# Performance work log

Measured on AMD Instinct MI355X. Metric: run time of the kernel, lower is better.

## Reference

```python
import jax, jax.numpy as jnp
import numpy as np

HEADS = 8
DIM_HEAD = 40
LN_EPS = 1e-5


def setup_inputs() -> dict:
    key = jax.random.key(0)
    ks = jax.random.split(key, 6)
    b, c, h, w = 8, 320, 64, 64
    ctx_len, ctx_dim = 77, 768
    inner = HEADS * DIM_HEAD  # 320
    return {
        "x": jax.random.normal(ks[0], (b, c, h, w), jnp.float32),
        "context": jax.random.normal(ks[1], (b, ctx_len, ctx_dim), jnp.float32),
        "Wq": jax.random.normal(ks[2], (c, inner), jnp.float32) * 0.02,
        "Wk": jax.random.normal(ks[3], (ctx_dim, inner), jnp.float32) * 0.02,
        "Wv": jax.random.normal(ks[4], (ctx_dim, inner), jnp.float32) * 0.02,
        "Wout": jax.random.normal(ks[5], (inner, c), jnp.float32) * 0.02,
        "bout": jnp.zeros((c,), jnp.float32),
        "gamma": jnp.ones((c,), jnp.float32),
        "beta": jnp.zeros((c,), jnp.float32),
    }


def reference(x, context, Wq, Wk, Wv, Wout, bout, gamma, beta):
    b, c, h, w = x.shape
    n = h * w
    scale = DIM_HEAD ** -0.5
    # flatten spatial -> tokens: [b, n, c]
    x_flat = x.reshape(b, c, n).transpose(0, 2, 1)
    # LayerNorm over channel dim
    mu = jnp.mean(x_flat, axis=-1, keepdims=True)
    var = jnp.mean((x_flat - mu) ** 2, axis=-1, keepdims=True)
    x_norm = (x_flat - mu) / jnp.sqrt(var + LN_EPS) * gamma + beta
    # projections (no bias), split heads: [b, h, n, d]
    def split_heads(t):
        bb, nn, _ = t.shape
        return t.reshape(bb, nn, HEADS, DIM_HEAD).transpose(0, 2, 1, 3)
    q = split_heads(x_norm @ Wq)
    k = split_heads(context @ Wk)
    v = split_heads(context @ Wv)
    sim = jnp.einsum("bhid,bhjd->bhij", q, k) * scale  # [b,H,n,ctx]
    attn = jax.nn.softmax(sim, axis=-1)
    out = jnp.einsum("bhij,bhjd->bhid", attn, v)
    out = out.transpose(0, 2, 1, 3).reshape(b, n, HEADS * DIM_HEAD)
    out = out @ Wout + bout  # dropout is identity at inference
    out = out + x_flat
    return out.transpose(0, 2, 1).reshape(b, c, h, w)
```

## Files before the change

kernel.cpp:

```cpp
#include <hip/hip_runtime.h>

#define HEADS 8
#define DH 40
constexpr int Bn   = 8;
constexpr int Cc   = 320;
constexpr int Nn   = 4096;
constexpr int CTX  = 77;
constexpr float LN_EPS = 1e-5f;
constexpr float SCALE  = 0.15811388300841897f;

typedef short bf16x8 __attribute__((ext_vector_type(8)));
typedef float f32x4  __attribute__((ext_vector_type(4)));
typedef unsigned short us;

__device__ inline us f2bf(float f) {
    unsigned u = __float_as_uint(f);
    u += 0x7fffu + ((u >> 16) & 1u);
    return (us)(u >> 16);
}
__device__ inline float bf2f(us h) {
    return __uint_as_float(((unsigned)h) << 16);
}

__global__ __launch_bounds__(256) void wtrans_all(const float* __restrict__ Wq,
                                                  const float* __restrict__ Wk,
                                                  const float* __restrict__ Wv,
                                                  const float* __restrict__ Wout,
                                                  us* __restrict__ wqF,
                                                  us* __restrict__ WkT,
                                                  us* __restrict__ WvT,
                                                  us* __restrict__ WoutT) {
    int id = blockIdx.x;
    if (id >= 580) {
        int wid = (id - 580) * 4 + (threadIdx.x >> 6);
        int lane = threadIdx.x & 63, lr = lane & 15, g = lane >> 4;
        int ct = wid / 10, kc = wid % 10;
        int k0 = kc * 32 + g * 8, co = ct * 16 + lr;
        us tmp[8];
        #pragma unroll
        for (int e = 0; e < 8; ++e)
            tmp[e] = f2bf(Wq[(size_t)(k0 + e) * 320 + co]);
        ((uint4*)wqF)[(size_t)wid * 64 + lane] = *(uint4*)tmp;
        return;
    }
    const float* in; us* out; int K, t;
    if (id < 240)      { in = Wk;   out = WkT;   K = 768; t = id; }
    else if (id < 480) { in = Wv;   out = WvT;   K = 768; t = id - 240; }
    else               { in = Wout; out = WoutT; K = 320; t = id - 480; }
    int ktiles = K >> 5;
    int kb = (t % ktiles) * 32, ob = (t / ktiles) * 32;

    __shared__ float tile[32][33];
    int tx = threadIdx.x & 31, ty = threadIdx.x >> 5;
    #pragma unroll
    for (int i = 0; i < 32; i += 8)
        tile[ty + i][tx] = in[(size_t)(kb + ty + i) * 320 + ob + tx];
    __syncthreads();
    #pragma unroll
    for (int i = 0; i < 32; i += 8)
        out[(size_t)(ob + ty + i) * K + kb + tx] = f2bf(tile[tx][ty + i]);
}

__global__ __launch_bounds__(256, 3) void ln_q_fused(const float* __restrict__ x,
                                                     const float* __restrict__ gamma,
                                                     const float* __restrict__ beta,
                                                     const us* __restrict__ wqF,
                                                     us* __restrict__ qG) {
    __shared__ __align__(16) us xnt[64 * 328];
    __shared__ float red1[4][64], red2[4][64];
    __shared__ float mu_s[64], rs_s[64];

    int b  = blockIdx.x >> 6;
    int t0 = (blockIdx.x & 63) * 64;
    int tid = threadIdx.x;
    int tl = tid & 63, cg = tid >> 6;
    const float* xb = x + (size_t)b * Cc * Nn + t0 + tl;

    float s1 = 0.f, s2 = 0.f;
    #pragma unroll 8
    for (int i = 0; i < 80; ++i) {
        int c = cg * 80 + i;
        float v = xb[(size_t)c * Nn];
        s1 += v; s2 += v * v;
        xnt[tl * 328 + c] = f2bf(v);
    }
    red1[cg][tl] = s1; red2[cg][tl] = s2;
    __syncthreads();
    if (tid < 64) {
        float a1 = red1[0][tl] + red1[1][tl] + red1[2][tl] + red1[3][tl];
        float a2 = red2[0][tl] + red2[1][tl] + red2[2][tl] + red2[3][tl];
        float mu = a1 * (1.0f / Cc);
        float var = a2 * (1.0f / Cc) - mu * mu;
        mu_s[tl] = mu; rs_s[tl] = rsqrtf(var + LN_EPS);
    }
    __syncthreads();
    float mu = mu_s[tl], rs = rs_s[tl];
    #pragma unroll 4
    for (int i = 0; i < 40; ++i) {
        int c = cg * 80 + i * 2;
        unsigned u = *(unsigned*)&xnt[tl * 328 + c];
        float v0 = bf2f((us)(u & 0xffff));
        float v1 = bf2f((us)(u >> 16));
        unsigned lo = f2bf((v0 - mu) * rs * gamma[c]     + beta[c]);
        unsigned hi = f2bf((v1 - mu) * rs * gamma[c + 1] + beta[c + 1]);
        *(unsigned*)&xnt[tl * 328 + c] = lo | (hi << 16);
    }
    __syncthreads();

    int lane = tid & 63, w = tid >> 6;
    int lr = lane & 15, g = lane >> 4;
    f32x4 acc[4][5] = {};
    const bf16x8* wq = (const bf16x8*)wqF;
    for (int kc = 0; kc < 10; ++kc) {
        bf16x8 bfr[5];
        #pragma unroll
        for (int nt = 0; nt < 5; ++nt)
            bfr[nt] = wq[(size_t)((w * 5 + nt) * 10 + kc) * 64 + lane];
        bf16x8 afr[4];
        #pragma unroll
        for (int mt = 0; mt < 4; ++mt)
            afr[mt] = *(const bf16x8*)&xnt[(mt * 16 + lr) * 328 + kc * 32 + g * 8];
        #pragma unroll
        for (int mt = 0; mt < 4; ++mt)
            #pragma unroll
            for (int nt = 0; nt < 5; ++nt)
                acc[mt][nt] = __builtin_amdgcn_mfma_f32_16x16x32_bf16(afr[mt], bfr[nt], acc[mt][nt], 0, 0, 0);
    }
    __syncthreads();

    #pragma unroll
    for (int mt = 0; mt < 4; ++mt)
        #pragma unroll
        for (int nt = 0; nt < 5; ++nt)
            #pragma unroll
            for (int r = 0; r < 4; ++r)
                xnt[(mt * 16 + g * 4 + r) * 328 + w * 80 + nt * 16 + lr] = f2bf(acc[mt][nt][r]);
    __syncthreads();

    size_t gtb = (size_t)b * 256 + (blockIdx.x & 63) * 4;
    #pragma unroll
    for (int it = 0; it < 10; ++it) {
        int f_lin = it * 4 + w;
        int tile = f_lin / 10, f = f_lin % 10;
        uint4 v = *(uint4*)&xnt[(tile * 16 + lr) * 328 + f * 32 + g * 8];
        ((uint4*)qG)[((gtb + tile) * 10 + f) * 64 + lane] = v;
    }
}

__global__ __launch_bounds__(256) void gemm_kv(const float* __restrict__ ctx,
                                               const us* __restrict__ WkT,
                                               const us* __restrict__ WvT,
                                               us* __restrict__ kbuf,
                                               us* __restrict__ vbuf) {
    const us* Bt = blockIdx.z ? WvT : WkT;
    us* Cm = blockIdx.z ? vbuf : kbuf;
    constexpr int K = 768, M = 616;
    __shared__ __align__(16) char Al[64 * 128];
    __shared__ __align__(16) char Bl[64 * 128];
    int m0 = blockIdx.x * 64;
    int n0 = blockIdx.y * 64;
    int tid = threadIdx.x;
    int lane = tid & 63, wave = tid >> 6;
    int wm = (wave >> 1) * 32, wn = (wave & 1) * 32;

    f32x4 acc[2][2] = {};

    for (int kc = 0; kc < K; kc += 64) {
        #pragma unroll
        for (int i = 0; i < 2; ++i) {
            int chunk = tid + 256 * i;
            int r = chunk >> 3, c8 = chunk & 7;
            int off = (r * 128 + c8 * 16) ^ ((r & 7) << 4);
            int gr = m0 + r;
            uint4 av = make_uint4(0, 0, 0, 0);
            if (gr < M) {
                float4 f0 = *(const float4*)(ctx + (size_t)gr * K + kc + c8 * 8);
                float4 f1 = *(const float4*)(ctx + (size_t)gr * K + kc + c8 * 8 + 4);
                av.x = f2bf(f0.x) | ((unsigned)f2bf(f0.y) << 16);
                av.y = f2bf(f0.z) | ((unsigned)f2bf(f0.w) << 16);
                av.z = f2bf(f1.x) | ((unsigned)f2bf(f1.y) << 16);
                av.w = f2bf(f1.z) | ((unsigned)f2bf(f1.w) << 16);
            }
            *(uint4*)(Al + off) = av;
            *(uint4*)(Bl + off) = *(const uint4*)(Bt + (size_t)(n0 + r) * K + kc + c8 * 8);
        }
        __syncthreads();

        #pragma unroll
        for (int kk = 0; kk < 64; kk += 32) {
            bf16x8 a[2], bfr[2];
            int lr = lane & 15;
            int lkb = (kk + (lane >> 4) * 8) * 2;
            #pragma unroll
            for (int mi = 0; mi < 2; ++mi) {
                int row = wm + mi * 16 + lr;
                a[mi] = *(const bf16x8*)(Al + ((row * 128 + lkb) ^ ((row & 7) << 4)));
            }
            #pragma unroll
            for (int ni = 0; ni < 2; ++ni) {
                int row = wn + ni * 16 + lr;
                bfr[ni] = *(const bf16x8*)(Bl + ((row * 128 + lkb) ^ ((row & 7) << 4)));
            }
            #pragma unroll
            for (int mi = 0; mi < 2; ++mi)
                #pragma unroll
                for (int ni = 0; ni < 2; ++ni)
                    acc[mi][ni] = __builtin_amdgcn_mfma_f32_16x16x32_bf16(a[mi], bfr[ni], acc[mi][ni], 0, 0, 0);
        }
        __syncthreads();
    }

    int lr = lane & 15, lq = lane >> 4;
    #pragma unroll
    for (int mi = 0; mi < 2; ++mi)
        #pragma unroll
        for (int ni = 0; ni < 2; ++ni)
            #pragma unroll
            for (int r = 0; r < 4; ++r) {
                int row = m0 + wm + mi * 16 + lq * 4 + r;
                int col = n0 + wn + ni * 16 + lr;
                if (row < M)
                    Cm[(size_t)row * 320 + col] = f2bf(acc[mi][ni][r]);
            }
}

__global__ __launch_bounds__(256) void gemm_vw(const us* __restrict__ WoutT,
                                               const us* __restrict__ vbuf,
                                               us* __restrict__ vwT) {
    int b = blockIdx.z, h = blockIdx.y, cb = blockIdx.x * 64;
    int tid = threadIdx.x, lane = tid & 63, w = tid >> 6;
    int lr = lane & 15, g = lane >> 4;

    int crow = cb + w * 16 + lr;
    const us* ab = WoutT + (size_t)crow * 320 + h * DH;
    bf16x8 a0 = *(const bf16x8*)(ab + g * 8);
    bf16x8 a1 = {};
    if (g == 0) a1 = *(const bf16x8*)(ab + 32);

    f32x4 acc[5] = {};
    #pragma unroll
    for (int nt = 0; nt < 5; ++nt) {
        int j = nt * 16 + lr;
        bool jv = j < CTX;
        const us* kr = vbuf + (size_t)(b * CTX + (jv ? j : 0)) * 320 + h * DH;
        bf16x8 b0 = {}, b1 = {};
        if (jv) b0 = *(const bf16x8*)(kr + g * 8);
        if (jv && g == 0) b1 = *(const bf16x8*)(kr + 32);
        acc[nt] = __builtin_amdgcn_mfma_f32_16x16x32_bf16(a0, b0, acc[nt], 0, 0, 0);
        acc[nt] = __builtin_amdgcn_mfma_f32_16x16x32_bf16(a1, b1, acc[nt], 0, 0, 0);
    }

    #pragma unroll
    for (int nt = 0; nt < 5; ++nt)
        #pragma unroll
        for (int r = 0; r < 4; ++r) {
            int c = cb + w * 16 + g * 4 + r;
            float val = (nt == 4 && lr >= 13) ? 0.f : acc[nt][r];
            vwT[((size_t)(b * 320 + c)) * 640 + h * 80 + nt * 16 + lr] = f2bf(val);
        }
}

__global__ __launch_bounds__(256) void repack_all(const us* __restrict__ kbuf,
                                                  const us* __restrict__ vwT,
                                                  us* __restrict__ kF,
                                                  us* __restrict__ vwF) {
    int id = blockIdx.x;
    int lane = threadIdx.x & 63, lr = lane & 15, g = lane >> 4;
    if (id < 160) {
        int wid = id * 4 + (threadIdx.x >> 6);
        int kc = wid & 1, nt = (wid >> 1) % 5, h = (wid / 10) & 7, b = wid / 80;
        int j = nt * 16 + lr, d0 = kc * 32 + g * 8;
        bf16x8 v = {};
        if (j < CTX && d0 < DH)
            v = *(const bf16x8*)(kbuf + ((size_t)(b * CTX + j)) * 320 + h * DH + d0);
        ((bf16x8*)kF)[(size_t)wid * 64 + lane] = v;
    } else {
        int wid = (id - 160) * 4 + (threadIdx.x >> 6);
        int mi = wid % 5, ks = (wid / 5) % 20, w = (wid / 100) & 3, b = wid / 400;
        int co = w * 80 + mi * 16 + lr, k = ks * 32 + g * 8;
        bf16x8 v = *(const bf16x8*)(vwT + ((size_t)(b * 320 + co)) * 640 + k);
        ((bf16x8*)vwF)[(size_t)wid * 64 + lane] = v;
    }
}

__global__ __launch_bounds__(256, 2) void attn_out(const us* __restrict__ qG,
                                                   const us* __restrict__ kF,
                                                   const us* __restrict__ vwF,
                                                   const float* __restrict__ bout,
                                                   const float* __restrict__ x,
                                                   float* __restrict__ out) {
    __shared__ __align__(16) char Pl[64 * 640];

    int bid = blockIdx.x;
    int b = bid & 7, ts = bid >> 3;
    int t0 = ts * 64;
    int tid = threadIdx.x, lane = tid & 63, w = tid >> 6;
    int lr = lane & 15, g = lane >> 4;

    const bf16x8* qfb = (const bf16x8*)qG;
    const bf16x8* kfb = (const bf16x8*)kF;

    f32x4 o[5][4] = {};

    #pragma unroll
    for (int p = 0; p < 2; ++p) {
        int h = p * 4 + w;
        size_t kfh = (size_t)((b * 8 + h) * 10) * 64;
        bf16x8 kb0[5], kb1[5];
        #pragma unroll
        for (int nt = 0; nt < 5; ++nt) {
            kb0[nt] = kfb[kfh + (nt * 2 + 0) * 64 + lane];
            kb1[nt] = kfb[kfh + (nt * 2 + 1) * 64 + lane];
        }
        int f0 = (5 * h + g) >> 2, l0 = ((5 * h + g) & 3) * 16 + lr;
        int f1 = (5 * h + 4) >> 2, l1 = ((5 * h + 4) & 3) * 16 + lr;

        #pragma unroll
        for (int mt = 0; mt < 4; ++mt) {
            const bf16x8* qt = qfb + (size_t)(b * 256 + ts * 4 + mt) * 640;
            bf16x8 a0 = qt[f0 * 64 + l0];
            bf16x8 a1 = {};
            if (g == 0) a1 = qt[f1 * 64 + l1];

            f32x4 S[5] = {};
            #pragma unroll
            for (int nt = 0; nt < 5; ++nt) {
                S[nt] = __builtin_amdgcn_mfma_f32_16x16x32_bf16(a0, kb0[nt], S[nt], 0, 0, 0);
                S[nt] = __builtin_amdgcn_mfma_f32_16x16x32_bf16(a1, kb1[nt], S[nt], 0, 0, 0);
            }

            float pv[5][4];
            #pragma unroll
            for (int nt = 0; nt < 5; ++nt)
                #pragma unroll
                for (int r = 0; r < 4; ++r)
                    pv[nt][r] = (nt == 4 && lr >= 13) ? 0.f : __expf(S[nt][r] * SCALE);
            #pragma unroll
            for (int r = 0; r < 4; ++r) {
                float su = pv[0][r] + pv[1][r] + pv[2][r] + pv[3][r] + pv[4][r];
                #pragma unroll
                for (int off = 1; off < 16; off <<= 1)
                    su += __shfl_xor(su, off);
                float inv = 1.0f / su;
                int row = mt * 16 + g * 4 + r;
                #pragma unroll
                for (int nt = 0; nt < 5; ++nt)
                    *(us*)(Pl + ((row * 640 + (w * 80 + nt * 16 + lr) * 2) ^ ((row & 7) << 4))) =
                        f2bf(pv[nt][r] * inv);
            }
        }
        __syncthreads();

        const bf16x8* vwb = (const bf16x8*)vwF + (size_t)(((b * 4 + w) * 20 + p * 10) * 5) * 64 + lane;
        __builtin_amdgcn_s_setprio(1);
        for (int ks = 0; ks < 10; ++ks) {
            bf16x8 av[5];
            #pragma unroll
            for (int mi = 0; mi < 5; ++mi)
                av[mi] = vwb[(ks * 5 + mi) * 64];
            bf16x8 pb[4];
            #pragma unroll
            for (int nt = 0; nt < 4; ++nt) {
                int row = nt * 16 + lr;
                pb[nt] = *(const bf16x8*)(Pl + ((row * 640 + ks * 64 + g * 16) ^ ((row & 7) << 4)));
            }
            #pragma unroll
            for (int mi = 0; mi < 5; ++mi)
                #pragma unroll
                for (int nt = 0; nt < 4; ++nt)
                    o[mi][nt] = __builtin_amdgcn_mfma_f32_16x16x32_bf16(av[mi], pb[nt], o[mi][nt], 0, 0, 0);
        }
        __builtin_amdgcn_s_setprio(0);
        __syncthreads();
    }

    int cw = w * 80;
    #pragma unroll
    for (int mi = 0; mi < 5; ++mi)
        #pragma unroll
        for (int r = 0; r < 4; ++r) {
            int co = cw + mi * 16 + g * 4 + r;
            float bo = bout[co];
            #pragma unroll
            for (int nt = 0; nt < 4; ++nt) {
                size_t oi = ((size_t)(b * 320 + co)) * 4096 + t0 + nt * 16 + lr;
                out[oi] = o[mi][nt][r] + bo + x[oi];
            }
        }
}

extern "C" void kernel_launch(void* const* d_in, const int* in_sizes, int n_in,
                              void* d_out, int out_size, void* d_ws, size_t ws_size,
                              hipStream_t stream) {
    const float* x     = (const float*)d_in[0];
    const float* ctx   = (const float*)d_in[1];
    const float* Wq    = (const float*)d_in[2];
    const float* Wk    = (const float*)d_in[3];
    const float* Wv    = (const float*)d_in[4];
    const float* Wout  = (const float*)d_in[5];
    const float* bout  = (const float*)d_in[6];
    const float* gamma = (const float*)d_in[7];
    const float* beta  = (const float*)d_in[8];
    float* out = (float*)d_out;
    char* ws = (char*)d_ws;

    us* qG    = (us*)(ws);
    us* kbuf  = (us*)(ws + 20971520);
    us* vbuf  = (us*)(ws + 21365760);
    us* vwT   = (us*)(ws + 21760000);
    us* vwF   = (us*)(ws + 25036800);
    us* kF    = (us*)(ws + 28313600);
    us* wqF   = (us*)(ws + 28968960);
    us* WkT   = (us*)(ws + 29173760);
    us* WvT   = (us*)(ws + 29665280);
    us* WoutT = (us*)(ws + 30156800);

    wtrans_all<<<dim3(630), 256, 0, stream>>>(Wq, Wk, Wv, Wout, wqF, WkT, WvT, WoutT);
    gemm_kv<<<dim3(10, 5, 2), 256, 0, stream>>>(ctx, WkT, WvT, kbuf, vbuf);
    gemm_vw<<<dim3(5, 8, 8), 256, 0, stream>>>(WoutT, vbuf, vwT);
    repack_all<<<dim3(960), 256, 0, stream>>>(kbuf, vwT, kF, vwF);
    ln_q_fused<<<dim3(512), 256, 0, stream>>>(x, gamma, beta, wqF, qG);
    attn_out<<<dim3(512), 256, 0, stream>>>(qG, kF, vwF, bout, x, out);
}
```

Measured before the change: 96.88 us.

## Use 8 waves per block in attn_out with split-K output reduction via LDS

The attention kernel now launches 512 threads, so all 8 heads compute softmax probabilities at once into a larger 80KB LDS buffer instead of doing two sequential head passes. The output GEMM is split across wave pairs along K, and partial sums are exchanged through shared memory before the bias and residual epilogue. This is meant to raise parallelism and remove one pass and its barriers. In exchange it uses more LDS per block, which may cap occupancy, and adds a reduction step with extra syncs.

```diff
diff --git a/kernel.cpp b/kernel.cpp
--- a/kernel.cpp
+++ b/kernel.cpp
@@ -283,13 +283,13 @@
     }
 }
 
-__global__ __launch_bounds__(256, 2) void attn_out(const us* __restrict__ qG,
+__global__ __launch_bounds__(512, 4) void attn_out(const us* __restrict__ qG,
                                                    const us* __restrict__ kF,
                                                    const us* __restrict__ vwF,
                                                    const float* __restrict__ bout,
                                                    const float* __restrict__ x,
                                                    float* __restrict__ out) {
-    __shared__ __align__(16) char Pl[64 * 640];
+    __shared__ __align__(16) char smem[81920];
 
     int bid = blockIdx.x;
     int b = bid & 7, ts = bid >> 3;
@@ -299,12 +299,10 @@
 
     const bf16x8* qfb = (const bf16x8*)qG;
     const bf16x8* kfb = (const bf16x8*)kF;
-
-    f32x4 o[5][4] = {};
-
-    #pragma unroll
-    for (int p = 0; p < 2; ++p) {
-        int h = p * 4 + w;
+    char* Pl = smem;
+
+    {
+        int h = w;
         size_t kfh = (size_t)((b * 8 + h) * 10) * 64;
         bf16x8 kb0[5], kb1[5];
         #pragma unroll
@@ -345,44 +343,61 @@
                 int row = mt * 16 + g * 4 + r;
                 #pragma unroll
                 for (int nt = 0; nt < 5; ++nt)
-                    *(us*)(Pl + ((row * 640 + (w * 80 + nt * 16 + lr) * 2) ^ ((row & 7) << 4))) =
+                    *(us*)(Pl + ((row * 1280 + (h * 80 + nt * 16 + lr) * 2) ^ ((row & 7) << 4))) =
                         f2bf(pv[nt][r] * inv);
             }
         }
-        __syncthreads();
-
-        const bf16x8* vwb = (const bf16x8*)vwF + (size_t)(((b * 4 + w) * 20 + p * 10) * 5) * 64 + lane;
-        __builtin_amdgcn_s_setprio(1);
-        for (int ks = 0; ks < 10; ++ks) {
-            bf16x8 av[5];
-            #pragma unroll
-            for (int mi = 0; mi < 5; ++mi)
-                av[mi] = vwb[(ks * 5 + mi) * 64];
-            bf16x8 pb[4];
-            #pragma unroll
-            for (int nt = 0; nt < 4; ++nt) {
-                int row = nt * 16 + lr;
-                pb[nt] = *(const bf16x8*)(Pl + ((row * 640 + ks * 64 + g * 16) ^ ((row & 7) << 4)));
-            }
-            #pragma unroll
-            for (int mi = 0; mi < 5; ++mi)
-                #pragma unroll
-                for (int nt = 0; nt < 4; ++nt)
-                    o[mi][nt] = __builtin_amdgcn_mfma_f32_16x16x32_bf16(av[mi], pb[nt], o[mi][nt], 0, 0, 0);
-        }
-        __builtin_amdgcn_s_setprio(0);
-        __syncthreads();
-    }
-
-    int cw = w * 80;
+    }
+    __syncthreads();
+
+    int wc = w >> 1, kh = w & 1;
+    f32x4 o[5][4] = {};
+    const bf16x8* vwb = (const bf16x8*)vwF + (size_t)((b * 4 + wc) * 100 + kh * 50) * 64 + lane;
+    __builtin_amdgcn_s_setprio(1);
+    for (int ks = 0; ks < 10; ++ks) {
+        bf16x8 av[5];
+        #pragma unroll
+        for (int mi = 0; mi < 5; ++mi)
+            av[mi] = vwb[(ks * 5 + mi) * 64];
+        bf16x8 pb[4];
+        #pragma unroll
+        for (int nt = 0; nt < 4; ++nt) {
+            int row = nt * 16 + lr;
+            pb[nt] = *(const bf16x8*)(Pl + ((row * 1280 + (kh * 10 + ks) * 64 + g * 16) ^ ((row & 7) << 4)));
+        }
+        #pragma unroll
+        for (int mi = 0; mi < 5; ++mi)
+            #pragma unroll
+            for (int nt = 0; nt < 4; ++nt)
+                o[mi][nt] = __builtin_amdgcn_mfma_f32_16x16x32_bf16(av[mi], pb[nt], o[mi][nt], 0, 0, 0);
+    }
+    __builtin_amdgcn_s_setprio(0);
+    __syncthreads();
+
+    f32x4* part = (f32x4*)smem;
+    int oth = 1 - kh;
     #pragma unroll
     for (int mi = 0; mi < 5; ++mi)
         #pragma unroll
-        for (int r = 0; r < 4; ++r) {
-            int co = cw + mi * 16 + g * 4 + r;
-            float bo = bout[co];
-            #pragma unroll
-            for (int nt = 0; nt < 4; ++nt) {
+        for (int ntl = 0; ntl < 2; ++ntl)
+            part[((wc * 2 + kh) * 10 + mi * 2 + ntl) * 64 + lane] = o[mi][oth * 2 + ntl];
+    __syncthreads();
+    #pragma unroll
+    for (int mi = 0; mi < 5; ++mi)
+        #pragma unroll
+        for (int ntl = 0; ntl < 2; ++ntl)
+            o[mi][kh * 2 + ntl] += part[((wc * 2 + oth) * 10 + mi * 2 + ntl) * 64 + lane];
+
+    int cw = wc * 80;
+    #pragma unroll
+    for (int mi = 0; mi < 5; ++mi)
+        #pragma unroll
+        for (int ntl = 0; ntl < 2; ++ntl) {
+            int nt = kh * 2 + ntl;
+            #pragma unroll
+            for (int r = 0; r < 4; ++r) {
+                int co = cw + mi * 16 + g * 4 + r;
+                float bo = bout[co];
                 size_t oi = ((size_t)(b * 320 + co)) * 4096 + t0 + nt * 16 + lr;
                 out[oi] = o[mi][nt][r] + bo + x[oi];
             }
@@ -420,5 +435,5 @@
     gemm_vw<<<dim3(5, 8, 8), 256, 0, stream>>>(WoutT, vbuf, vwT);
     repack_all<<<dim3(960), 256, 0, stream>>>(kbuf, vwT, kF, vwF);
     ln_q_fused<<<dim3(512), 256, 0, stream>>>(x, gamma, beta, wqF, qG);
-    attn_out<<<dim3(512), 256, 0, stream>>>(qG, kF, vwF, bout, x, out);
-}
+    attn_out<<<dim3(512), 512, 0, stream>>>(qG, kF, vwF, bout, x, out);
+}
```

Result: slower. 197.1 us (+103.5%).
